# Optimization experiments

Measured on AMD Instinct MI355X. Metric: run time of the kernel, lower is better.

The kernel has to match this reference:

```python
import jax, jax.numpy as jnp
import numpy as np

N_NODES = 50000
N_EDGES = 800000
D = 64  # in_dim == hidden_dim == out_dim
BN_EPS = 1e-5


def setup_inputs() -> dict:
    key = jax.random.key(0)
    ks = jax.random.split(key, 12)
    x = jax.random.normal(ks[0], (N_NODES, D), dtype=jnp.float32)
    edge_index = jax.random.randint(ks[1], (2, N_EDGES), 0, N_NODES, dtype=jnp.int64)
    scale = 1.0 / np.sqrt(D)
    W1 = jax.random.normal(ks[2], (D, D), dtype=jnp.float32) * scale
    b1 = jnp.zeros((D,), jnp.float32)
    W2 = jax.random.normal(ks[3], (D, D), dtype=jnp.float32) * scale
    b2 = jnp.zeros((D,), jnp.float32)
    W3 = jax.random.normal(ks[4], (D, D), dtype=jnp.float32) * scale
    b3 = jnp.zeros((D,), jnp.float32)
    # BatchNorm (eval mode: running stats) params for the two hidden layers
    g1 = jnp.ones((D,), jnp.float32); be1 = jnp.zeros((D,), jnp.float32)
    m1 = jax.random.normal(ks[5], (D,), dtype=jnp.float32) * 0.1
    v1 = jax.random.uniform(ks[6], (D,), dtype=jnp.float32, minval=0.5, maxval=1.5)
    g2 = jnp.ones((D,), jnp.float32); be2 = jnp.zeros((D,), jnp.float32)
    m2 = jax.random.normal(ks[7], (D,), dtype=jnp.float32) * 0.1
    v2 = jax.random.uniform(ks[8], (D,), dtype=jnp.float32, minval=0.5, maxval=1.5)
    return {"x": x, "edge_index": edge_index,
            "W1": W1, "b1": b1, "g1": g1, "be1": be1, "m1": m1, "v1": v1,
            "W2": W2, "b2": b2, "g2": g2, "be2": be2, "m2": m2, "v2": v2,
            "W3": W3, "b3": b3}


def reference(x, edge_index, W1, b1, g1, be1, m1, v1,
              W2, b2, g2, be2, m2, v2, W3, b3):
    N = x.shape[0]
    loop = jnp.arange(N, dtype=edge_index.dtype)
    src = jnp.concatenate([edge_index[0], loop])  # [E+N]
    dst = jnp.concatenate([edge_index[1], loop])
    # GCN symmetric normalization: deg over dst (with self loops)
    deg = jax.ops.segment_sum(jnp.ones(dst.shape, x.dtype), dst, num_segments=N)
    dinv = jnp.where(deg > 0, jax.lax.rsqrt(deg), 0.0)
    norm = (dinv[src] * dinv[dst])[:, None]  # [E+N, 1]

    def gcn_conv(h, W, b):
        h = h @ W  # linear transform first (PyG GCNConv order)
        return jax.ops.segment_sum(h[src] * norm, dst, num_segments=N) + b

    def bn(h, g, be, m, v):  # eval-mode BatchNorm1d
        return (h - m) * jax.lax.rsqrt(v + BN_EPS) * g + be

    h = jax.nn.relu(bn(gcn_conv(x, W1, b1), g1, be1, m1, v1))
    h = jax.nn.relu(bn(gcn_conv(h, W2, b2), g2, be2, m2, v2))
    return gcn_conv(h, W3, b3)
```

## Files before the change

### kernel.cpp

```cpp
#include <hip/hip_runtime.h>
#include <hip/hip_fp16.h>

#define D 64
#define BN_EPS 1e-5f
typedef unsigned short u16;
typedef unsigned int u32;

#define NB_MAX 256
#define A3_EDGES 4096

__global__ __launch_bounds__(256) void k_setup(
    const void* __restrict__ ei, int N, int* __restrict__ flag,
    int* __restrict__ bucketCnt,
    const float* __restrict__ g1, const float* __restrict__ be1,
    const float* __restrict__ m1, const float* __restrict__ v1,
    const float* __restrict__ g2, const float* __restrict__ be2,
    const float* __restrict__ m2, const float* __restrict__ v2,
    float* __restrict__ bn) {
    int d = threadIdx.x;
    bucketCnt[d] = 0;
    if (d < 64) {
        float s = g1[d] * rsqrtf(v1[d] + BN_EPS);
        bn[d] = s; bn[64 + d] = be1[d] - m1[d] * s;
        float q = g2[d] * rsqrtf(v2[d] + BN_EPS);
        bn[128 + d] = q; bn[192 + d] = be2[d] - m2[d] * q;
    } else if (d == 64) {
        const long long* p = (const long long*)ei;
        int ok = 1;
        for (int j = 0; j < 16; ++j) {
            long long v = p[j];
            if (v < 0 || v >= (long long)N) { ok = 0; break; }
        }
        *flag = ok;
    }
}

__device__ __forceinline__ int get_idx(const void* ei, int is64, int pos) {
    if (is64) return (int)((const long long*)ei)[pos];
    return ((const int*)ei)[pos];
}

__global__ __launch_bounds__(256) void k_bucket_count(
    const void* __restrict__ ei, const int* __restrict__ flag, int E, int nb,
    int* __restrict__ bucketCnt) {
    __shared__ int hist[NB_MAX];
    for (int i = threadIdx.x; i < nb; i += 256) hist[i] = 0;
    __syncthreads();
    const int is64 = *flag;
    for (int e = blockIdx.x * 256 + threadIdx.x; e < E; e += gridDim.x * 256)
        atomicAdd(&hist[get_idx(ei, is64, E + e) >> 8], 1);
    __syncthreads();
    for (int i = threadIdx.x; i < nb; i += 256)
        if (hist[i]) atomicAdd(&bucketCnt[i], hist[i]);
}

__global__ __launch_bounds__(256) void k_bucket_scan(
    const int* __restrict__ bucketCnt, int nb, int* __restrict__ bucketOff,
    int* __restrict__ bucketCur, int* __restrict__ rowptr, int N, int E) {
    __shared__ int s[256];
    int tid = threadIdx.x;
    int v = (tid < nb) ? bucketCnt[tid] : 0;
    s[tid] = v; __syncthreads();
    for (int off = 1; off < 256; off <<= 1) {
        int t = (tid >= off) ? s[tid - off] : 0;
        __syncthreads(); s[tid] += t; __syncthreads();
    }
    if (tid < nb) { bucketOff[tid] = s[tid] - v; bucketCur[tid] = 0; }
    if (tid == nb) bucketOff[nb] = E;
    if (tid == 0) rowptr[N] = E;
}

__global__ __launch_bounds__(256) void k_bucket_scatter(
    const void* __restrict__ ei, const int* __restrict__ flag, int E, int nb,
    const int* __restrict__ bucketOff, int* __restrict__ bucketCur,
    u32* __restrict__ staged) {
    __shared__ u32 recs[A3_EDGES];
    __shared__ int hist[NB_MAX];
    __shared__ int lpos[NB_MAX];
    __shared__ int gbase[NB_MAX];
    const int tid = threadIdx.x;
    const int base = blockIdx.x * A3_EDGES;
    const int cnt = min(A3_EDGES, E - base);
    const int is64 = *flag;
    for (int i = tid; i < nb; i += 256) hist[i] = 0;
    __syncthreads();
    u32 myrec[16];
    const int per = (cnt + 255) >> 8;
    for (int j = 0; j < per; ++j) {
        int o = j * 256 + tid;
        if (o < cnt) {
            int e = base + o;
            u32 src = (u32)get_idx(ei, is64, e);
            u32 dst = (u32)get_idx(ei, is64, E + e);
            u32 bkt = dst >> 8;
            myrec[j] = (bkt << 24) | (src << 8) | (dst & 255u);
            atomicAdd(&hist[bkt], 1);
        } else myrec[j] = 0xffffffffu;
    }
    __syncthreads();
    int v = (tid < nb) ? hist[tid] : 0;
    lpos[tid] = v; __syncthreads();
    for (int off = 1; off < 256; off <<= 1) {
        int t = (tid >= off) ? lpos[tid - off] : 0;
        __syncthreads(); lpos[tid] += t; __syncthreads();
    }
    int excl = lpos[tid] - v;
    if (tid < nb && v > 0) gbase[tid] = atomicAdd(&bucketCur[tid], v);
    __syncthreads();
    if (tid < nb) { lpos[tid] = excl; hist[tid] = 0; }
    __syncthreads();
    for (int j = 0; j < per; ++j) {
        u32 r = myrec[j];
        if (r != 0xffffffffu) {
            int b = (int)(r >> 24);
            int p = lpos[b] + atomicAdd(&hist[b], 1);
            recs[p] = r;
        }
    }
    __syncthreads();
    const int wave = tid >> 6, lane = tid & 63;
    for (int b = wave; b < nb; b += 4) {
        int c = hist[b]; if (!c) continue;
        int gdst = bucketOff[b] + gbase[b];
        int lsrc = lpos[b];
        for (int k = lane; k < c; k += 64) staged[gdst + k] = recs[lsrc + k];
    }
}

__global__ __launch_bounds__(256) void k_bucket_build(
    const u32* __restrict__ staged, const int* __restrict__ bucketOff,
    int* __restrict__ rowptr, float* __restrict__ dinv, u16* __restrict__ csr,
    int N) {
    __shared__ int hist[256], off[256], cur[256];
    const int b = blockIdx.x, tid = threadIdx.x;
    const int beg = bucketOff[b], end = bucketOff[b + 1];
    hist[tid] = 0;
    __syncthreads();
    for (int i = beg + tid; i < end; i += 256)
        atomicAdd(&hist[staged[i] & 255u], 1);
    __syncthreads();
    int v = hist[tid];
    off[tid] = v; __syncthreads();
    for (int o = 1; o < 256; o <<= 1) {
        int t = (tid >= o) ? off[tid - o] : 0;
        __syncthreads(); off[tid] += t; __syncthreads();
    }
    int excl = off[tid] - v;
    const int dst = b * 256 + tid;
    if (dst < N) { rowptr[dst] = beg + excl; dinv[dst] = rsqrtf(1.0f + (float)v); }
    __syncthreads();
    off[tid] = excl; cur[tid] = 0;
    __syncthreads();
    for (int i = beg + tid; i < end; i += 256) {
        u32 r = staged[i];
        int dl = (int)(r & 255u);
        int p = beg + off[dl] + atomicAdd(&cur[dl], 1);
        csr[p] = (u16)((r >> 8) & 0xffffu);
    }
}

#define GROWS 64
__global__ __launch_bounds__(256) void k_gemm(
    const float* __restrict__ h, const float* __restrict__ W,
    const float* __restrict__ dinv, __half* __restrict__ h2s, int N) {
    __shared__ float hs[GROWS * 65];
    __shared__ float Ws[64 * 64];
    const int tid = threadIdx.x;
    const int row0 = blockIdx.x * GROWS;
    const int nrow = min(GROWS, N - row0);
    const float4* Wp = (const float4*)W;
    float4* Wsp = (float4*)Ws;
    for (int i = tid; i < 1024; i += 256) Wsp[i] = Wp[i];
    const float4* hp = (const float4*)h + (size_t)row0 * 16;
    for (int i = tid; i < nrow * 16; i += 256) {
        float4 t = hp[i];
        int r = i >> 4, c4 = (i & 15) << 2;
        float* dp = &hs[r * 65 + c4];
        dp[0] = t.x; dp[1] = t.y; dp[2] = t.z; dp[3] = t.w;
    }
    __syncthreads();
    const int r = tid >> 2, q = tid & 3;
    const int row = row0 + r;
    if (r >= nrow) return;
    float out[16];
#pragma unroll
    for (int c = 0; c < 16; ++c) out[c] = 0.f;
    for (int k = 0; k < 64; ++k) {
        float a = hs[r * 65 + k];
        const float* Wk = &Ws[k * 64 + q * 16];
#pragma unroll
        for (int c = 0; c < 16; ++c) out[c] = fmaf(a, Wk[c], out[c]);
    }
    const float di = dinv[row];
    u32 pk[8];
#pragma unroll
    for (int c = 0; c < 8; ++c) {
        u32 lo = __half_as_ushort(__float2half(di * out[2 * c]));
        u32 hi = __half_as_ushort(__float2half(di * out[2 * c + 1]));
        pk[c] = (hi << 16) | lo;
    }
    uint4* op = (uint4*)(h2s + (size_t)row * 64 + q * 16);
    op[0] = make_uint4(pk[0], pk[1], pk[2], pk[3]);
    op[1] = make_uint4(pk[4], pk[5], pk[6], pk[7]);
}

__device__ __forceinline__ void acc8(float* acc, const float4& v) {
    const __half2* hv = (const __half2*)&v;
#pragma unroll
    for (int q2 = 0; q2 < 4; ++q2) {
        float2 t = __half22float2(hv[q2]);
        acc[2 * q2] += t.x; acc[2 * q2 + 1] += t.y;
    }
}

template <int MODE>
__global__ __launch_bounds__(256) void k_gather(
    const int* __restrict__ rowptr, const u16* __restrict__ csr,
    const __half* __restrict__ h2s, const float* __restrict__ dinv,
    const float* __restrict__ b, const float* __restrict__ bn, int bn_off,
    const float* __restrict__ Wn, __half* __restrict__ h2o,
    float* __restrict__ outp, int N, int E) {
    __shared__ float ytile[16][68];
    const int tid = threadIdx.x;
    const int lane = tid & 63;
    const int n16 = tid >> 4;
    const int node = blockIdx.x * 16 + n16;
    const int g2 = (lane >> 3) & 1;
    const int f = lane & 7;
    const int lbase = lane & ~15;

    float acc[8];
#pragma unroll
    for (int k = 0; k < 8; ++k) acc[k] = 0.f;

    if (node < N) {
        const int beg = rowptr[node], end = rowptr[node + 1];
        float4 sv = ((const float4*)(h2s + (size_t)node * 64))[f];
        if (g2 == 0) acc8(acc, sv);

        for (int c = beg; c < end; c += 16) {
            int p = c + (lane & 15);
            int idx = csr[p < E ? p : E - 1];
            const int navail = min(16, end - c);
            float4 v[8];
            int e[8];
#pragma unroll
            for (int j = 0; j < 8; ++j) {
                e[j] = 2 * j + g2;
                int s = __shfl(idx, lbase + e[j]);
                v[j] = ((const float4*)(h2s + (size_t)s * 64))[f];
            }
#pragma unroll
            for (int j = 0; j < 8; ++j)
                if (e[j] < navail) acc8(acc, v[j]);
        }
#pragma unroll
        for (int k = 0; k < 8; ++k) acc[k] += __shfl_xor(acc[k], 8);

        if (g2 == 0) {
            const float dn = dinv[node];
            float bb[8], y[8];
            ((float4*)bb)[0] = ((const float4*)b)[2 * f];
            ((float4*)bb)[1] = ((const float4*)b)[2 * f + 1];
#pragma unroll
            for (int k = 0; k < 8; ++k) y[k] = dn * acc[k] + bb[k];
            if (MODE == 0) {
                float ss[8], tt[8];
                ((float4*)ss)[0] = ((const float4*)(bn + bn_off))[2 * f];
                ((float4*)ss)[1] = ((const float4*)(bn + bn_off))[2 * f + 1];
                ((float4*)tt)[0] = ((const float4*)(bn + bn_off + 64))[2 * f];
                ((float4*)tt)[1] = ((const float4*)(bn + bn_off + 64))[2 * f + 1];
#pragma unroll
                for (int k = 0; k < 8; ++k) y[k] = fmaxf(y[k] * ss[k] + tt[k], 0.f);
                float4* yt = (float4*)&ytile[n16][f * 8];
                yt[0] = make_float4(y[0], y[1], y[2], y[3]);
                yt[1] = make_float4(y[4], y[5], y[6], y[7]);
            } else {
                float4* op = (float4*)(outp + (size_t)node * 64 + f * 8);
                op[0] = make_float4(y[0], y[1], y[2], y[3]);
                op[1] = make_float4(y[4], y[5], y[6], y[7]);
            }
        }
    }
    if (MODE == 0) {
        __syncthreads();
        if (node < N) {
            const int cq = (tid & 15) << 2;
            float z0 = 0.f, z1 = 0.f, z2 = 0.f, z3 = 0.f;
#pragma unroll 4
            for (int k = 0; k < 64; ++k) {
                float a = ytile[n16][k];
                float4 w = *(const float4*)(Wn + k * 64 + cq);
                z0 = fmaf(a, w.x, z0); z1 = fmaf(a, w.y, z1);
                z2 = fmaf(a, w.z, z2); z3 = fmaf(a, w.w, z3);
            }
            const float dn = dinv[node];
            u32 p0 = ((u32)__half_as_ushort(__float2half(dn * z1)) << 16)
                   | __half_as_ushort(__float2half(dn * z0));
            u32 p1 = ((u32)__half_as_ushort(__float2half(dn * z3)) << 16)
                   | __half_as_ushort(__float2half(dn * z2));
            *(uint2*)(h2o + (size_t)node * 64 + cq) = make_uint2(p0, p1);
        }
    }
}

extern "C" void kernel_launch(void* const* d_in, const int* in_sizes, int n_in,
                              void* d_out, int out_size, void* d_ws, size_t ws_size,
                              hipStream_t stream) {
    const float* x  = (const float*)d_in[0];
    const void*  ei = d_in[1];
    const float* W1 = (const float*)d_in[2];
    const float* b1 = (const float*)d_in[3];
    const float* g1 = (const float*)d_in[4];
    const float* be1= (const float*)d_in[5];
    const float* m1 = (const float*)d_in[6];
    const float* v1 = (const float*)d_in[7];
    const float* W2 = (const float*)d_in[8];
    const float* b2 = (const float*)d_in[9];
    const float* g2 = (const float*)d_in[10];
    const float* be2= (const float*)d_in[11];
    const float* m2 = (const float*)d_in[12];
    const float* v2 = (const float*)d_in[13];
    const float* W3 = (const float*)d_in[14];
    const float* b3 = (const float*)d_in[15];

    const int N = in_sizes[0] / D;
    const int E = in_sizes[1] / 2;
    const int nb = (N + 255) >> 8;
    float* out = (float*)d_out;

    char* ws = (char*)d_ws;
    int*   flag      = (int*)ws;
    float* bn        = (float*)(ws + 256);
    int*   bucketCnt = (int*)(ws + 2048);
    int*   bucketOff = (int*)(ws + 4096);
    int*   bucketCur = (int*)(ws + 8192);
    int*   rowptr    = (int*)(ws + 12288);
    float* dinv      = (float*)(ws + 12288 + 200192);
    u32*   staged    = (u32*)(ws + 12288 + 2 * 200192);
    u16*   csr       = (u16*)((char*)staged + (size_t)E * 4 + 256);
    __half* bufA     = (__half*)((char*)csr + (size_t)E * 2 + 256);
    __half* bufC     = bufA + (size_t)N * D;

    const int gGemm = (N + GROWS - 1) / GROWS;
    const int gGath = (N + 15) / 16;
    const int gA3   = (E + A3_EDGES - 1) / A3_EDGES;

    k_setup<<<1, 256, 0, stream>>>(ei, N, flag, bucketCnt,
                                   g1, be1, m1, v1, g2, be2, m2, v2, bn);
    k_bucket_count<<<256, 256, 0, stream>>>(ei, flag, E, nb, bucketCnt);
    k_bucket_scan<<<1, 256, 0, stream>>>(bucketCnt, nb, bucketOff, bucketCur,
                                         rowptr, N, E);
    k_bucket_scatter<<<gA3, 256, 0, stream>>>(ei, flag, E, nb, bucketOff,
                                              bucketCur, staged);
    k_bucket_build<<<nb, 256, 0, stream>>>(staged, bucketOff, rowptr, dinv, csr, N);

    k_gemm<<<gGemm, 256, 0, stream>>>(x, W1, dinv, bufA, N);
    k_gather<0><<<gGath, 256, 0, stream>>>(rowptr, csr, bufA, dinv, b1, bn, 0,
                                           W2, bufC, nullptr, N, E);
    k_gather<0><<<gGath, 256, 0, stream>>>(rowptr, csr, bufC, dinv, b2, bn, 128,
                                           W3, bufA, nullptr, N, E);
    k_gather<1><<<gGath, 256, 0, stream>>>(rowptr, csr, bufA, dinv, b3, bn, 0,
                                           nullptr, nullptr, out, N, E);
}
```

Baseline: 165.9 us.

## Split feature matrix into two half-planes and gather each plane separately

Stores the fp16 transformed features as two 32-column planes of N×32, so each gather pass works on a half-width table that is more likely to stay in cache. Each layer's gather is split into two launches. The first writes its post-BN half to a scratch buffer, and the second reloads it and does the fused next-layer GEMM. Loads now use 4 lanes per row with 32 edges per iteration, and stores are nontemporal. This adds kernel launches, re-reads the CSR index per plane and adds a scratch round-trip.

```diff
diff --git a/kernel.cpp b/kernel.cpp
--- a/kernel.cpp
+++ b/kernel.cpp
@@ -5,6 +5,9 @@
 #define BN_EPS 1e-5f
 typedef unsigned short u16;
 typedef unsigned int u32;
+typedef u32   __attribute__((ext_vector_type(2))) u32x2;
+typedef u32   __attribute__((ext_vector_type(4))) u32x4;
+typedef float __attribute__((ext_vector_type(4))) f32x4;
 
 #define NB_MAX 256
 #define A3_EDGES 4096
@@ -199,9 +202,13 @@
         u32 hi = __half_as_ushort(__float2half(di * out[2 * c + 1]));
         pk[c] = (hi << 16) | lo;
     }
-    uint4* op = (uint4*)(h2s + (size_t)row * 64 + q * 16);
-    op[0] = make_uint4(pk[0], pk[1], pk[2], pk[3]);
-    op[1] = make_uint4(pk[4], pk[5], pk[6], pk[7]);
+    __half* bp = h2s + (size_t)(q >> 1) * ((size_t)N * 32)
+               + (size_t)row * 32 + (q & 1) * 16;
+    u32x4* op = (u32x4*)bp;
+    u32x4 o0 = {pk[0], pk[1], pk[2], pk[3]};
+    u32x4 o1 = {pk[4], pk[5], pk[6], pk[7]};
+    __builtin_nontemporal_store(o0, op);
+    __builtin_nontemporal_store(o1, op + 1);
 }
 
 __device__ __forceinline__ void acc8(float* acc, const float4& v) {
@@ -213,20 +220,26 @@
     }
 }
 
-template <int MODE>
-__global__ __launch_bounds__(256) void k_gather(
+template <int ROLE>
+__global__ __launch_bounds__(256) void k_gather_h(
     const int* __restrict__ rowptr, const u16* __restrict__ csr,
-    const __half* __restrict__ h2s, const float* __restrict__ dinv,
-    const float* __restrict__ b, const float* __restrict__ bn, int bn_off,
-    const float* __restrict__ Wn, __half* __restrict__ h2o,
-    float* __restrict__ outp, int N, int E) {
+    const __half* __restrict__ plane, const float* __restrict__ dinv,
+    const float* __restrict__ bias,
+    const float* __restrict__ bnS,
+    const float* __restrict__ bnT,
+    __half* __restrict__ z0,
+    const float* __restrict__ Wn,
+    __half* __restrict__ h2o,
+    float* __restrict__ outp, int outoff,
+    int N, int E) {
     __shared__ float ytile[16][68];
     const int tid = threadIdx.x;
     const int lane = tid & 63;
     const int n16 = tid >> 4;
     const int node = blockIdx.x * 16 + n16;
-    const int g2 = (lane >> 3) & 1;
-    const int f = lane & 7;
+    const int s = (lane >> 2) & 3;
+    const int f = lane & 3;
+    const int l16 = lane & 15;
     const int lbase = lane & ~15;
 
     float acc[8];
@@ -235,71 +248,111 @@
 
     if (node < N) {
         const int beg = rowptr[node], end = rowptr[node + 1];
-        float4 sv = ((const float4*)(h2s + (size_t)node * 64))[f];
-        if (g2 == 0) acc8(acc, sv);
-
-        for (int c = beg; c < end; c += 16) {
-            int p = c + (lane & 15);
-            int idx = csr[p < E ? p : E - 1];
-            const int navail = min(16, end - c);
-            float4 v[8];
-            int e[8];
-#pragma unroll
-            for (int j = 0; j < 8; ++j) {
-                e[j] = 2 * j + g2;
-                int s = __shfl(idx, lbase + e[j]);
-                v[j] = ((const float4*)(h2s + (size_t)s * 64))[f];
-            }
-#pragma unroll
-            for (int j = 0; j < 8; ++j)
-                if (e[j] < navail) acc8(acc, v[j]);
-        }
-#pragma unroll
-        for (int k = 0; k < 8; ++k) acc[k] += __shfl_xor(acc[k], 8);
-
-        if (g2 == 0) {
+        if (s == 0) acc8(acc, ((const float4*)(plane + (size_t)node * 32))[f]);
+        for (int c = beg; c < end; c += 32) {
+            int pA = c + l16, pB = pA + 16;
+            int iA = csr[pA < E ? pA : E - 1];
+            int iB = csr[pB < E ? pB : E - 1];
+            float4 vA[4], vB[4];
+#pragma unroll
+            for (int j = 0; j < 4; ++j) {
+                int sA = __shfl(iA, lbase + 4 * j + s);
+                vA[j] = ((const float4*)(plane + (size_t)sA * 32))[f];
+            }
+#pragma unroll
+            for (int j = 0; j < 4; ++j) {
+                int sB = __shfl(iB, lbase + 4 * j + s);
+                vB[j] = ((const float4*)(plane + (size_t)sB * 32))[f];
+            }
+            const int navail = end - c;
+#pragma unroll
+            for (int j = 0; j < 4; ++j) if (4 * j + s < navail) acc8(acc, vA[j]);
+#pragma unroll
+            for (int j = 0; j < 4; ++j) if (16 + 4 * j + s < navail) acc8(acc, vB[j]);
+        }
+#pragma unroll
+        for (int k = 0; k < 8; ++k) {
+            acc[k] += __shfl_xor(acc[k], 4);
+            acc[k] += __shfl_xor(acc[k], 8);
+        }
+
+        if (s == 0) {
             const float dn = dinv[node];
-            float bb[8], y[8];
-            ((float4*)bb)[0] = ((const float4*)b)[2 * f];
-            ((float4*)bb)[1] = ((const float4*)b)[2 * f + 1];
-#pragma unroll
-            for (int k = 0; k < 8; ++k) y[k] = dn * acc[k] + bb[k];
-            if (MODE == 0) {
-                float ss[8], tt[8];
-                ((float4*)ss)[0] = ((const float4*)(bn + bn_off))[2 * f];
-                ((float4*)ss)[1] = ((const float4*)(bn + bn_off))[2 * f + 1];
-                ((float4*)tt)[0] = ((const float4*)(bn + bn_off + 64))[2 * f];
-                ((float4*)tt)[1] = ((const float4*)(bn + bn_off + 64))[2 * f + 1];
-#pragma unroll
-                for (int k = 0; k < 8; ++k) y[k] = fmaxf(y[k] * ss[k] + tt[k], 0.f);
-                float4* yt = (float4*)&ytile[n16][f * 8];
-                yt[0] = make_float4(y[0], y[1], y[2], y[3]);
-                yt[1] = make_float4(y[4], y[5], y[6], y[7]);
+            float y[8];
+            float4 b0 = *(const float4*)(bias + 8 * f);
+            float4 b1 = *(const float4*)(bias + 8 * f + 4);
+#pragma unroll
+            for (int k = 0; k < 4; ++k) {
+                y[k] = dn * acc[k] + (&b0.x)[k];
+                y[4 + k] = dn * acc[4 + k] + (&b1.x)[k];
+            }
+            if (ROLE == 2) {
+                float* op = outp + (size_t)node * 64 + outoff + 8 * f;
+                f32x4 y0 = {y[0], y[1], y[2], y[3]};
+                f32x4 y1 = {y[4], y[5], y[6], y[7]};
+                __builtin_nontemporal_store(y0, (f32x4*)op);
+                __builtin_nontemporal_store(y1, (f32x4*)op + 1);
             } else {
-                float4* op = (float4*)(outp + (size_t)node * 64 + f * 8);
-                op[0] = make_float4(y[0], y[1], y[2], y[3]);
-                op[1] = make_float4(y[4], y[5], y[6], y[7]);
-            }
-        }
-    }
-    if (MODE == 0) {
+                float4 s0 = *(const float4*)(bnS + 8 * f);
+                float4 s1 = *(const float4*)(bnS + 8 * f + 4);
+                float4 t0 = *(const float4*)(bnT + 8 * f);
+                float4 t1 = *(const float4*)(bnT + 8 * f + 4);
+                float z[8];
+#pragma unroll
+                for (int k = 0; k < 4; ++k) {
+                    z[k] = fmaxf(y[k] * (&s0.x)[k] + (&t0.x)[k], 0.f);
+                    z[4 + k] = fmaxf(y[4 + k] * (&s1.x)[k] + (&t1.x)[k], 0.f);
+                }
+                if (ROLE == 0) {
+                    u32 pk[4];
+#pragma unroll
+                    for (int k = 0; k < 4; ++k) {
+                        u32 lo = __half_as_ushort(__float2half(z[2 * k]));
+                        u32 hi = __half_as_ushort(__float2half(z[2 * k + 1]));
+                        pk[k] = (hi << 16) | lo;
+                    }
+                    u32x4 zo = {pk[0], pk[1], pk[2], pk[3]};
+                    __builtin_nontemporal_store(
+                        zo, (u32x4*)(z0 + (size_t)node * 32 + 8 * f));
+                } else {
+                    float4* yt = (float4*)&ytile[n16][32 + 8 * f];
+                    yt[0] = make_float4(z[0], z[1], z[2], z[3]);
+                    yt[1] = make_float4(z[4], z[5], z[6], z[7]);
+                }
+            }
+        } else if (ROLE == 1 && s == 1) {
+            u32x4 zv = __builtin_nontemporal_load(
+                (const u32x4*)(z0 + (size_t)node * 32 + 8 * f));
+            u32 w[4] = {zv.x, zv.y, zv.z, zv.w};
+            float* yt = &ytile[n16][8 * f];
+#pragma unroll
+            for (int k = 0; k < 4; ++k) {
+                float2 t = __half22float2(*(__half2*)&w[k]);
+                yt[2 * k] = t.x; yt[2 * k + 1] = t.y;
+            }
+        }
+    }
+    if (ROLE == 1) {
         __syncthreads();
         if (node < N) {
             const int cq = (tid & 15) << 2;
-            float z0 = 0.f, z1 = 0.f, z2 = 0.f, z3 = 0.f;
+            float z0v = 0.f, z1v = 0.f, z2v = 0.f, z3v = 0.f;
 #pragma unroll 4
             for (int k = 0; k < 64; ++k) {
                 float a = ytile[n16][k];
                 float4 w = *(const float4*)(Wn + k * 64 + cq);
-                z0 = fmaf(a, w.x, z0); z1 = fmaf(a, w.y, z1);
-                z2 = fmaf(a, w.z, z2); z3 = fmaf(a, w.w, z3);
+                z0v = fmaf(a, w.x, z0v); z1v = fmaf(a, w.y, z1v);
+                z2v = fmaf(a, w.z, z2v); z3v = fmaf(a, w.w, z3v);
             }
             const float dn = dinv[node];
-            u32 p0 = ((u32)__half_as_ushort(__float2half(dn * z1)) << 16)
-                   | __half_as_ushort(__float2half(dn * z0));
-            u32 p1 = ((u32)__half_as_ushort(__float2half(dn * z3)) << 16)
-                   | __half_as_ushort(__float2half(dn * z2));
-            *(uint2*)(h2o + (size_t)node * 64 + cq) = make_uint2(p0, p1);
+            u32 p0 = ((u32)__half_as_ushort(__float2half(dn * z1v)) << 16)
+                   | __half_as_ushort(__float2half(dn * z0v));
+            u32 p1 = ((u32)__half_as_ushort(__float2half(dn * z3v)) << 16)
+                   | __half_as_ushort(__float2half(dn * z2v));
+            __half* bp = h2o + (size_t)(cq >> 5) * ((size_t)N * 32)
+                       + (size_t)node * 32 + (cq & 31);
+            u32x2 zo = {p0, p1};
+            __builtin_nontemporal_store(zo, (u32x2*)bp);
         }
     }
 }
@@ -327,6 +380,7 @@
     const int N = in_sizes[0] / D;
     const int E = in_sizes[1] / 2;
     const int nb = (N + 255) >> 8;
+    const size_t Nh = (size_t)N * 32;
     float* out = (float*)d_out;
 
     char* ws = (char*)d_ws;
@@ -339,8 +393,9 @@
     float* dinv      = (float*)(ws + 12288 + 200192);
     u32*   staged    = (u32*)(ws + 12288 + 2 * 200192);
     u16*   csr       = (u16*)((char*)staged + (size_t)E * 4 + 256);
-    __half* bufA     = (__half*)((char*)csr + (size_t)E * 2 + 256);
-    __half* bufC     = bufA + (size_t)N * D;
+    __half* z0buf    = (__half*)((char*)csr + (size_t)E * 2 + 256);
+    __half* bufA     = z0buf + Nh;
+    __half* bufC     = bufA + 2 * Nh;
 
     const int gGemm = (N + GROWS - 1) / GROWS;
     const int gGath = (N + 15) / 16;
@@ -356,10 +411,19 @@
     k_bucket_build<<<nb, 256, 0, stream>>>(staged, bucketOff, rowptr, dinv, csr, N);
 
     k_gemm<<<gGemm, 256, 0, stream>>>(x, W1, dinv, bufA, N);
-    k_gather<0><<<gGath, 256, 0, stream>>>(rowptr, csr, bufA, dinv, b1, bn, 0,
-                                           W2, bufC, nullptr, N, E);
-    k_gather<0><<<gGath, 256, 0, stream>>>(rowptr, csr, bufC, dinv, b2, bn, 128,
-                                           W3, bufA, nullptr, N, E);
-    k_gather<1><<<gGath, 256, 0, stream>>>(rowptr, csr, bufA, dinv, b3, bn, 0,
-                                           nullptr, nullptr, out, N, E);
-}
+
+    k_gather_h<0><<<gGath, 256, 0, stream>>>(rowptr, csr, bufA, dinv,
+        b1, bn, bn + 64, z0buf, nullptr, nullptr, nullptr, 0, N, E);
+    k_gather_h<1><<<gGath, 256, 0, stream>>>(rowptr, csr, bufA + Nh, dinv,
+        b1 + 32, bn + 32, bn + 96, z0buf, W2, bufC, nullptr, 0, N, E);
+
+    k_gather_h<0><<<gGath, 256, 0, stream>>>(rowptr, csr, bufC, dinv,
+        b2, bn + 128, bn + 192, z0buf, nullptr, nullptr, nullptr, 0, N, E);
+    k_gather_h<1><<<gGath, 256, 0, stream>>>(rowptr, csr, bufC + Nh, dinv,
+        b2 + 32, bn + 160, bn + 224, z0buf, W3, bufA, nullptr, 0, N, E);
+
+    k_gather_h<2><<<gGath, 256, 0, stream>>>(rowptr, csr, bufA, dinv,
+        b3, nullptr, nullptr, nullptr, nullptr, nullptr, out, 0, N, E);
+    k_gather_h<2><<<gGath, 256, 0, stream>>>(rowptr, csr, bufA + Nh, dinv,
+        b3 + 32, nullptr, nullptr, nullptr, nullptr, nullptr, out, 32, N, E);
+}
```

New measurement: 197.0 us. 18.7% more time.
